# Kernel tuning notes

Measured on AMD Instinct MI355X. Metric: run time of the kernel, lower is better.

The kernel has to match this reference:

```python
import jax, jax.numpy as jnp
import numpy as np

B, N, D, H = 512, 200, 128, 8
DH = D // H
CLIP = 10.0
NEG = -1e9


def setup_inputs():
    ks = jax.random.split(jax.random.key(0), 10)
    s = 1.0 / float(np.sqrt(D))
    f32 = jnp.float32
    return {
        "x": jax.random.normal(ks[0], (2, B, N, N), f32),
        "rf": jax.random.uniform(ks[1], (B, 2), f32),
        "node_embeddings": jax.random.normal(ks[2], (B, N, D), f32),
        "graph_embedding": jax.random.normal(ks[3], (B, D), f32),
        "Wk1_w": jax.random.normal(ks[4], (D, D), f32) * s,
        "Wk1_b": jnp.zeros((D,), f32),
        "Wv_w": jax.random.normal(ks[5], (D, D), f32) * s,
        "Wk2_w": jax.random.normal(ks[6], (D, D), f32) * s,
        "Wout_w": jax.random.normal(ks[7], (D, D), f32) * s,
        "Wq_w": jax.random.normal(ks[8], (D, D + 2), f32) * s,
        "init_node": jnp.zeros((D,), f32),
    }


def _forward(x, rf, node_embeddings, Wk1_w, Wk1_b, Wv_w, Wk2_w, Wout_w, Wq_w, init_node):
    # static projections (compute_static)
    K1 = node_embeddings @ Wk1_w.T + Wk1_b  # [B,N,D]
    V = node_embeddings @ Wv_w.T
    K2 = node_embeddings @ Wk2_w.T
    K1h = K1.reshape(B, N, H, DH).transpose(0, 2, 1, 3)  # [B,H,N,DH]
    Vh = V.reshape(B, N, H, DH).transpose(0, 2, 1, 3)
    barange = jnp.arange(B)
    narange = jnp.arange(N)

    def step(carry, _):
        mask, ctx, end = carry  # mask [B,N] bool, ctx [B,2+D], end [B] bool
        Q1 = ctx @ Wq_w.T  # [B,D]  (Wq_step)
        qh = Q1.reshape(B, H, DH)
        scores = jnp.einsum('bhd,bhnd->bhn', qh, K1h) / jnp.sqrt(jnp.float32(DH))
        scores = jnp.where(mask[:, None, :], NEG, scores)
        attn = jax.nn.softmax(scores, axis=-1)
        mha = jnp.einsum('bhn,bhnd->bhd', attn, Vh).reshape(B, D)
        Q2 = mha @ Wout_w.T  # [B,D]
        logits = CLIP * jnp.tanh(jnp.einsum('bd,bnd->bn', Q2, K2) / jnp.sqrt(jnp.float32(D)))
        logits = jnp.where(mask, NEG, logits)
        log_p = jax.nn.log_softmax(logits, axis=-1)  # [B,N]
        nxt = jnp.argmax(log_p, axis=-1)  # greedy decode (deterministic)
        nxt = jnp.where(end, nxt, 0)  # once node 0 chosen, stay at 0
        cur_emb = node_embeddings[barange, nxt]  # [B,D]
        end = end & (nxt != 0)
        mask = mask | (narange[None, :] == nxt[:, None])
        ctx = jnp.concatenate([rf, cur_emb], axis=1)
        return (mask, ctx, end), (log_p, nxt)

    ctx0 = jnp.concatenate([rf, jnp.broadcast_to(init_node, (B, D))], axis=1)
    carry0 = (jnp.zeros((B, N), bool), ctx0, jnp.ones((B,), bool))
    _, (log_ps, tours) = jax.lax.scan(step, carry0, None, length=N)
    log_ps = log_ps.transpose(1, 0, 2)  # [B,N,N]
    pi = tours.T  # [B,N]

    # get_cost
    index = jnp.argmax(pi == 0, axis=1)  # first occurrence of stop node 0
    steps_mask = narange[None, :] < index[:, None]
    cols = pi * steps_mask
    sol = jnp.zeros((B, N), jnp.float32).at[barange[:, None], cols].set(1.0)
    f1 = jnp.einsum('bn,bnm,bm->b', sol, x[0], sol)[:, None, None]  # [B,1,1]
    f2 = jnp.einsum('bn,bnm,bm->b', sol, x[1], sol)[:, None, None]
    cost = -(f1 * rf[0, 0] + f2 * rf[0, 1]).squeeze()  # [B]

    # log-likelihood of tour, weighted by solution membership
    chosen = jnp.take_along_axis(log_ps, pi[:, :, None], axis=2)[:, :, 0]  # [B,N]
    w = jnp.take_along_axis(sol, pi, axis=1)
    ll = jnp.sum(chosen * w, axis=1)  # [B]
    return cost, f1, f2, ll, pi


def reference(x, rf, node_embeddings, graph_embedding, Wk1_w, Wk1_b, Wv_w, Wk2_w, Wout_w, Wq_w, init_node):
    return _forward(x, rf, node_embeddings, Wk1_w, Wk1_b, Wv_w, Wk2_w, Wout_w, Wq_w, init_node)
```

## Files before the change

### kernel.cpp

```cpp
#include <hip/hip_runtime.h>
#include <math.h>

#define NEGV (-1e9f)

#define OUT_F   0l
#define M_F     52428800l
#define QR_F    (M_F + 65536l)
#define QI_F    (QR_F + 65536l)
#define SOL_F   (QI_F + 65536l)
#define WS_FLOATS (SOL_F + 102400l)

typedef float f32x4 __attribute__((ext_vector_type(4)));

#define DPPF(x, ctrl, oldv) __int_as_float(__builtin_amdgcn_update_dpp( \
      __float_as_int(oldv), __float_as_int(x), ctrl, 0xF, 0xF, false))

__device__ __forceinline__ float wave_max(float x) {
  x = fmaxf(x, DPPF(x, 0x111, -INFINITY));
  x = fmaxf(x, DPPF(x, 0x112, -INFINITY));
  x = fmaxf(x, DPPF(x, 0x114, -INFINITY));
  x = fmaxf(x, DPPF(x, 0x118, -INFINITY));
  x = fmaxf(x, DPPF(x, 0x142, -INFINITY));
  x = fmaxf(x, DPPF(x, 0x143, -INFINITY));
  return __int_as_float(__builtin_amdgcn_readlane(__float_as_int(x), 63));
}
__device__ __forceinline__ float wave_sum(float x) {
  x = x + DPPF(x, 0x111, 0.f);
  x = x + DPPF(x, 0x112, 0.f);
  x = x + DPPF(x, 0x114, 0.f);
  x = x + DPPF(x, 0x118, 0.f);
  x = x + DPPF(x, 0x142, 0.f);
  x = x + DPPF(x, 0x143, 0.f);
  return __int_as_float(__builtin_amdgcn_readlane(__float_as_int(x), 63));
}

__global__ __launch_bounds__(256)
void build_M(const float* __restrict__ Wk1, const float* __restrict__ Wv,
             const float* __restrict__ Wk2, const float* __restrict__ Wout,
             const float* __restrict__ Wq, float* __restrict__ Mbuf) {
  int g = blockIdx.x * 256 + threadIdx.x;
  int j = g >> 9, c = g & 511;
  float val;
  if (c < 128) {
    val = Wk1[c * 128 + j];
  } else if (c < 256) {
    val = Wv[(c - 128) * 128 + j];
  } else if (c < 384) {
    int d = c - 256;
    float s = 0.f;
    for (int e = 0; e < 128; ++e) s += Wk2[e * 128 + j] * Wout[e * 128 + d];
    val = s;
  } else {
    val = Wq[(c - 384) * 130 + 2 + j];
  }
  Mbuf[j * 512 + c] = val;
}

__global__ __launch_bounds__(256)
void build_Q(const float* __restrict__ rf, const float* __restrict__ Wq,
             const float* __restrict__ initn, float* __restrict__ QR,
             float* __restrict__ QI, int* __restrict__ ctr) {
  int g = blockIdx.x * 256 + threadIdx.x;
  if (g == 0) *ctr = 0;
  int b = g >> 7, d = g & 127;
  float qr = Wq[d * 130 + 0] * rf[b * 2 + 0] + Wq[d * 130 + 1] * rf[b * 2 + 1];
  float qi = qr;
  for (int j = 0; j < 128; ++j) qi += Wq[d * 130 + 2 + j] * initn[j];
  QR[g] = qr;
  QI[g] = qi;
}

__global__ __launch_bounds__(256)
void gemm_static(const float* __restrict__ emb, const float* __restrict__ Mbuf,
                 const float* __restrict__ bk1, const float* __restrict__ QR,
                 float* __restrict__ OUT) {
  int bid = blockIdx.x;
  int lo = bid & 7, hi = bid >> 3;
  int rt = lo + 8 * (hi % 200);
  int ct = hi / 200;
  int r0 = rt * 64, c0 = ct * 64;
  int t = threadIdx.x, ty = t >> 4, tx = t & 15;
  int row0 = r0 + ty * 4;
  int col  = c0 + tx * 4;
  float acc[4][4] = {};
  const float* mp = Mbuf + col;
  for (int kb = 0; kb < 32; ++kb) {
    int k = kb * 4;
    float4 b0 = *(const float4*)(mp + (long)(k + 0) * 512);
    float4 b1 = *(const float4*)(mp + (long)(k + 1) * 512);
    float4 b2 = *(const float4*)(mp + (long)(k + 2) * 512);
    float4 b3 = *(const float4*)(mp + (long)(k + 3) * 512);
    float bm[4][4] = {{b0.x,b0.y,b0.z,b0.w},{b1.x,b1.y,b1.z,b1.w},
                      {b2.x,b2.y,b2.z,b2.w},{b3.x,b3.y,b3.z,b3.w}};
    #pragma unroll
    for (int rr = 0; rr < 4; ++rr) {
      float4 a4 = *(const float4*)(emb + (long)(row0 + rr) * 128 + k);
      float av[4] = {a4.x, a4.y, a4.z, a4.w};
      #pragma unroll
      for (int i = 0; i < 4; ++i)
        #pragma unroll
        for (int cc = 0; cc < 4; ++cc)
          acc[rr][cc] += av[i] * bm[i][cc];
    }
  }
  float badd[4] = {0.f, 0.f, 0.f, 0.f};
  if (c0 < 128) {
    #pragma unroll
    for (int cc = 0; cc < 4; ++cc) badd[cc] = bk1[col + cc];
  }
  #pragma unroll
  for (int rr = 0; rr < 4; ++rr) {
    int row = row0 + rr;
    float v[4];
    #pragma unroll
    for (int cc = 0; cc < 4; ++cc) v[cc] = acc[rr][cc] + badd[cc];
    if (col >= 384) {
      int bb = row / 200;
      #pragma unroll
      for (int cc = 0; cc < 4; ++cc) v[cc] += QR[bb * 128 + (col - 384) + cc];
    }
    float4 v4; v4.x = v[0]; v4.y = v[1]; v4.z = v[2]; v4.w = v[3];
    *(float4*)(OUT + (long)row * 512 + col) = v4;
  }
}

__global__ void init_ctr(int* __restrict__ c) { *c = 0; }

__global__ __attribute__((amdgpu_flat_work_group_size(512, 512), amdgpu_waves_per_eu(2, 2)))
void decode512(const float* __restrict__ OUT, const float* __restrict__ QI,
               const float* __restrict__ x, const float* __restrict__ rf,
               int* __restrict__ ctr, float* __restrict__ out) {
  __shared__ __align__(16) float qall[201 * 128];
  __shared__ float sc[1600];
  __shared__ __align__(16) float mhal[128];
  __shared__ float lg[200];
  __shared__ float sb[200];
  __shared__ float redc[16];
  __shared__ int bsel;

  const int t = threadIdx.x;
  const int lane = t & 63, wave = t >> 6;
  const int o = t >> 2, r4 = t & 3;
  const int mn = t >> 1, half = t & 1;
  const int vst  = (r4 == 0) ? 0 : (r4 == 1 ? 48 : (r4 == 2 ? 100 : 152));
  const bool mid = (r4 == 1) || (r4 == 2);

  float kreg[64], ureg[64], vreg[52];

  for (;;) {
    if (t == 0) bsel = atomicAdd(ctr, 1);
    __syncthreads();
    const int b = bsel;
    if (b >= 512) break;
    const float* outb = OUT + (long)b * 200 * 512;

    for (int f = t; f < 25728; f += 512) {
      int row = f >> 7, d = f & 127;
      qall[f] = (row < 200) ? outb[row * 512 + 384 + d] : QI[b * 128 + d];
    }
    #pragma unroll
    for (int k = 0; k < 4; ++k) {
      int n = lane + 64 * k;
      if (n < 200) {
        const float* kp = outb + n * 512 + wave * 16;
        #pragma unroll
        for (int c = 0; c < 4; ++c)
          *(f32x4*)&kreg[k * 16 + c * 4] = *(const f32x4*)(kp + c * 4);
      } else {
        #pragma unroll
        for (int c = 0; c < 16; ++c) kreg[k * 16 + c] = 0.f;
      }
    }
    if (t < 400) {
      const float* up = outb + mn * 512 + 256 + 64 * half;
      #pragma unroll
      for (int c = 0; c < 16; ++c)
        *(f32x4*)&ureg[c * 4] = *(const f32x4*)(up + c * 4);
    }
    {
      const float* vp = outb + 128 + o;
      #pragma unroll
      for (int i = 0; i < 48; ++i) vreg[i] = vp[(vst + i) * 512];
      vreg[48] = mid ? vp[(vst + 48) * 512] : 0.f;
      vreg[49] = mid ? vp[(vst + 49) * 512] : 0.f;
      vreg[50] = mid ? vp[(vst + 50) * 512] : 0.f;
      vreg[51] = mid ? vp[(vst + 51) * 512] : 0.f;
    }

    int cur = 200;
    int mk = 0;
    bool cmb = false;
    bool live = true, picked0 = false;
    float llsum = 0.f, chose = 0.f;

    __syncthreads();

    for (int st = 0; st < 200; ++st) {
      {
        const float* qb = qall + cur * 128 + wave * 16;
        f32x4 q0 = *(const f32x4*)(qb + 0);
        f32x4 q1 = *(const f32x4*)(qb + 4);
        f32x4 q2 = *(const f32x4*)(qb + 8);
        f32x4 q3 = *(const f32x4*)(qb + 12);
        float sv[4];
        float mx = -INFINITY;
        #pragma unroll
        for (int k = 0; k < 4; ++k) {
          int n = lane + 64 * k;
          float s = -INFINITY;
          if (n < 200) {
            float a = q0[0] * kreg[k * 16 + 0];
            a += q0[1] * kreg[k * 16 + 1];
            a += q0[2] * kreg[k * 16 + 2];
            a += q0[3] * kreg[k * 16 + 3];
            a += q1[0] * kreg[k * 16 + 4];
            a += q1[1] * kreg[k * 16 + 5];
            a += q1[2] * kreg[k * 16 + 6];
            a += q1[3] * kreg[k * 16 + 7];
            a += q2[0] * kreg[k * 16 + 8];
            a += q2[1] * kreg[k * 16 + 9];
            a += q2[2] * kreg[k * 16 + 10];
            a += q2[3] * kreg[k * 16 + 11];
            a += q3[0] * kreg[k * 16 + 12];
            a += q3[1] * kreg[k * 16 + 13];
            a += q3[2] * kreg[k * 16 + 14];
            a += q3[3] * kreg[k * 16 + 15];
            s = a * 0.25f;
            if (mk & (1 << k)) s = NEGV;
          }
          sv[k] = s;
          mx = fmaxf(mx, s);
        }
        float vmax = wave_max(mx);
        float ls = 0.f;
        #pragma unroll
        for (int k = 0; k < 4; ++k) { sv[k] = expf(sv[k] - vmax); ls += sv[k]; }
        ls = wave_sum(ls);
        #pragma unroll
        for (int k = 0; k < 4; ++k) {
          int n = lane + 64 * k;
          if (n < 200) sc[wave * 200 + n] = sv[k] / ls;
        }
      }

      {
        const float* ap = sc + wave * 200 + vst;
        float ac[4] = {0.f, 0.f, 0.f, 0.f};
        #pragma unroll
        for (int c = 0; c < 12; ++c) {
          f32x4 av = *(const f32x4*)(ap + c * 4);
          float s = av[0] * vreg[c * 4 + 0];
          s += av[1] * vreg[c * 4 + 1];
          s += av[2] * vreg[c * 4 + 2];
          s += av[3] * vreg[c * 4 + 3];
          ac[c & 3] += s;
        }
        if (mid) {
          f32x4 av = *(const f32x4*)(ap + 48);
          float s = av[0] * vreg[48];
          s += av[1] * vreg[49]; s += av[2] * vreg[50]; s += av[3] * vreg[51];
          ac[0] += s;
        }
        float a = (ac[0] + ac[1]) + (ac[2] + ac[3]);
        a += DPPF(a, 0xB1, 0.f);
        a += DPPF(a, 0x4E, 0.f);
        if (r4 == 0) mhal[o] = a;
      }
      __syncthreads();

      if (t < 400) {
        float ac[4] = {0.f, 0.f, 0.f, 0.f};
        #pragma unroll
        for (int c = 0; c < 16; ++c) {
          f32x4 mh = *(const f32x4*)&mhal[64 * half + c * 4];
          float s = mh[0] * ureg[c * 4 + 0];
          s += mh[1] * ureg[c * 4 + 1];
          s += mh[2] * ureg[c * 4 + 2];
          s += mh[3] * ureg[c * 4 + 3];
          ac[c & 3] += s;
        }
        float a = (ac[0] + ac[1]) + (ac[2] + ac[3]);
        a += DPPF(a, 0xB1, 0.f);
        if (half == 0) {
          float l = 10.f * tanhf(a / 11.313708498984761f);
          lg[mn] = cmb ? NEGV : l;
        }
      }
      __syncthreads();

      int nxt;
      {
        float lv[4];
        float mx = -INFINITY;
        #pragma unroll
        for (int k = 0; k < 4; ++k) {
          int n = lane + 64 * k;
          lv[k] = (n < 200) ? lg[n] : -INFINITY;
          mx = fmaxf(mx, lv[k]);
        }
        float vmax = wave_max(mx);
        int bidx = -1;
        #pragma unroll
        for (int k = 0; k < 4; ++k) {
          unsigned long long bm =
              __ballot((lane + 64 * k < 200) && (lv[k] == vmax));
          if (bidx < 0 && bm != 0ull) bidx = k * 64 + (int)__builtin_ctzll(bm);
        }
        nxt = live ? bidx : 0;
        if (wave == 7) {
          float e = 0.f;
          #pragma unroll
          for (int k = 0; k < 4; ++k) e += expf(lv[k] - vmax);
          float se_ = wave_sum(e);
          float lse = logf(se_);
          if (t == 448) {
            chose = live ? (-lse) : ((lv[0] - vmax) - lse);
            out[2048 + (long)b * 200 + st] = (float)nxt;
          }
        }
      }

      if (!live) {
        if (t == 448) llsum += chose * (float)(200 - st);
        for (int s2 = st + 1 + t; s2 < 200; s2 += 512)
          out[2048 + (long)b * 200 + s2] = 0.f;
        break;
      }
      if (t == 448) llsum += chose;
      if ((nxt & 63) == lane) mk |= 1 << (nxt >> 6);
      if (t < 400 && nxt == mn) cmb = true;
      cur = nxt;
      if (nxt == 0) { live = false; picked0 = true; }
    }

    if (t == 448) out[1536 + b] = picked0 ? llsum : 0.f;
    if (t < 400 && half == 0) {
      float s = (mn == 0) ? 1.f : ((picked0 && cmb) ? 1.f : 0.f);
      sb[mn] = s;
    }
    __syncthreads();

    {
      const int c2 = t >> 1, hf = t & 1;
      float a1 = 0.f, a2 = 0.f;
      if (c2 < 200) {
        const float* xp0 = x + (long)b * 40000 + hf * 20000 + c2;
        const float* xp1 = x + 20480000l + (long)b * 40000 + hf * 20000 + c2;
        #pragma unroll 4
        for (int i = 0; i < 100; ++i) {
          float w2 = sb[hf * 100 + i];
          a1 += xp0[i * 200] * w2;
          a2 += xp1[i * 200] * w2;
        }
      }
      a1 += DPPF(a1, 0xB1, 0.f);
      a2 += DPPF(a2, 0xB1, 0.f);
      if (hf == 0 && c2 < 200) {
        float w = sb[c2];
        a1 *= w; a2 *= w;
      } else {
        a1 = 0.f; a2 = 0.f;
      }
      a1 = wave_sum(a1);
      a2 = wave_sum(a2);
      if (lane == 0) { redc[wave * 2] = a1; redc[wave * 2 + 1] = a2; }
      __syncthreads();
      if (t == 0) {
        float f1 = ((redc[0] + redc[2]) + (redc[4] + redc[6])) +
                   ((redc[8] + redc[10]) + (redc[12] + redc[14]));
        float f2 = ((redc[1] + redc[3]) + (redc[5] + redc[7])) +
                   ((redc[9] + redc[11]) + (redc[13] + redc[15]));
        out[b]        = -(f1 * rf[0] + f2 * rf[1]);
        out[512 + b]  = f1;
        out[1024 + b] = f2;
      }
    }
    __syncthreads();
  }
}

__global__ __attribute__((amdgpu_flat_work_group_size(1024, 1024)))
void decode(const float* __restrict__ OUT, const float* __restrict__ QI,
            int* __restrict__ ctr, float* __restrict__ sol,
            float* __restrict__ out) {
  __shared__ __align__(16) float k1r[25600];
  __shared__ __align__(16) float at[1600];
  __shared__ __align__(16) float mhal[128];
  __shared__ float lg[200];
  __shared__ __align__(16) float qv[128];
  __shared__ __align__(16) float ul[12800];
  __shared__ int   bci;
  __shared__ int   bsel;

  const int t = threadIdx.x;
  const int lane = t & 63, wave = t >> 6;
  const int o = t >> 3, q8 = t & 7;
  const int m4 = t >> 2, j4 = t & 3;
  const int stq = (q8 * 25) & ~3;
  const int cq  = ((((q8 + 1) * 25) & ~3) - stq) >> 2;

  for (;;) {
    if (t == 0) bsel = atomicAdd(ctr, 1);
    __syncthreads();
    const int b = bsel;
    if (b >= 512) break;
    const float* outb = OUT + (long)b * 200 * 512;

    for (int p = 0; p < 25; ++p) {
      int f = p * 1024 + t;
      int n = f >> 7, d = f & 127;
      k1r[n * 128 + ((d + 4 * n) & 127)] = outb[n * 512 + d];
    }
    for (int f = t; f < 12800; f += 1024) {
      int m = f >> 6, c = f & 63;
      ul[m * 64 + ((c + 4 * m) & 63)] =
          outb[m * 512 + 256 + (c >> 4) * 32 + 16 + (c & 15)];
    }
    f32x4 vA = {}, vB = {}, vC = {}, vD = {}, vE = {}, vF = {}, vG = {};
    {
      const float* vp = outb + 128 + o;
      #pragma unroll
      for (int e = 0; e < 4; ++e) vA[e] = vp[(stq + 0 + e) * 512];
      #pragma unroll
      for (int e = 0; e < 4; ++e) vB[e] = vp[(stq + 4 + e) * 512];
      #pragma unroll
      for (int e = 0; e < 4; ++e) vC[e] = vp[(stq + 8 + e) * 512];
      #pragma unroll
      for (int e = 0; e < 4; ++e) vD[e] = vp[(stq + 12 + e) * 512];
      #pragma unroll
      for (int e = 0; e < 4; ++e) vE[e] = vp[(stq + 16 + e) * 512];
      #pragma unroll
      for (int e = 0; e < 4; ++e) vF[e] = vp[(stq + 20 + e) * 512];
      if (cq == 7) {
        #pragma unroll
        for (int e = 0; e < 4; ++e) vG[e] = vp[(stq + 24 + e) * 512];
      }
    }
    f32x4 urR0 = {}, urR1 = {}, urR2 = {}, urR3 = {};
    if (t < 800) {
      const float* up = outb + m4 * 512 + 256 + j4 * 32;
      urR0 = *(const f32x4*)(up + 4 * ((0 + j4) & 3));
      urR1 = *(const f32x4*)(up + 4 * ((1 + j4) & 3));
      urR2 = *(const f32x4*)(up + 4 * ((2 + j4) & 3));
      urR3 = *(const f32x4*)(up + 4 * ((3 + j4) & 3));
    }
    if (t < 128) qv[t] = QI[b * 128 + t];

    int mk = 0;
    bool cm = false;
    bool live = true, picked0 = false;
    float llsum = 0.f, chose = 0.f;

    __syncthreads();

    for (int st = 0; st < 200; ++st) {
      if (wave < 8) {
        const int hb = wave * 16;
        float acc[4] = {};
        #pragma unroll
        for (int hf = 0; hf < 2; ++hf) {
          f32x4 qa = *(const f32x4*)&qv[hb + hf * 8];
          f32x4 qb2 = *(const f32x4*)&qv[hb + hf * 8 + 4];
          #pragma unroll
          for (int k = 0; k < 4; ++k) {
            int n = lane + 64 * k;
            if (n < 200) {
              const float* kb = k1r + n * 128;
              int off  = (hb + hf * 8 + 4 * n) & 127;
              int off2 = (hb + hf * 8 + 4 + 4 * n) & 127;
              f32x4 kA = *(const f32x4*)(kb + off);
              f32x4 kB = *(const f32x4*)(kb + off2);
              float ah = qa[0] * kA[0];
              ah += qa[1] * kA[1]; ah += qa[2] * kA[2]; ah += qa[3] * kA[3];
              ah += qb2[0] * kB[0]; ah += qb2[1] * kB[1];
              ah += qb2[2] * kB[2]; ah += qb2[3] * kB[3];
              acc[k] += ah;
            }
          }
        }
        float sv[4];
        float mx = -INFINITY;
        #pragma unroll
        for (int k = 0; k < 4; ++k) {
          int n = lane + 64 * k;
          float s = -INFINITY;
          if (n < 200) {
            s = acc[k] * 0.25f;
            if (mk & (1 << k)) s = NEGV;
          }
          sv[k] = s;
          mx = fmaxf(mx, s);
        }
        float vmax = wave_max(mx);
        float ls = 0.f;
        #pragma unroll
        for (int k = 0; k < 4; ++k) { sv[k] = expf(sv[k] - vmax); ls += sv[k]; }
        ls = wave_sum(ls);
        #pragma unroll
        for (int k = 0; k < 4; ++k) {
          int n = lane + 64 * k;
          if (n < 200) at[wave * 200 + n] = sv[k] / ls;
        }
      }
      __syncthreads();

      {
        const int h2 = t >> 7;
        const float* ap = at + h2 * 200 + stq;
        float a = 0.f;
        f32x4 av;
        av = *(const f32x4*)(ap + 0);
        a += av[0]*vA[0]; a += av[1]*vA[1]; a += av[2]*vA[2]; a += av[3]*vA[3];
        av = *(const f32x4*)(ap + 4);
        a += av[0]*vB[0]; a += av[1]*vB[1]; a += av[2]*vB[2]; a += av[3]*vB[3];
        av = *(const f32x4*)(ap + 8);
        a += av[0]*vC[0]; a += av[1]*vC[1]; a += av[2]*vC[2]; a += av[3]*vC[3];
        av = *(const f32x4*)(ap + 12);
        a += av[0]*vD[0]; a += av[1]*vD[1]; a += av[2]*vD[2]; a += av[3]*vD[3];
        av = *(const f32x4*)(ap + 16);
        a += av[0]*vE[0]; a += av[1]*vE[1]; a += av[2]*vE[2]; a += av[3]*vE[3];
        av = *(const f32x4*)(ap + 20);
        a += av[0]*vF[0]; a += av[1]*vF[1]; a += av[2]*vF[2]; a += av[3]*vF[3];
        if (cq == 7) {
          av = *(const f32x4*)(ap + 24);
          a += av[0]*vG[0]; a += av[1]*vG[1]; a += av[2]*vG[2]; a += av[3]*vG[3];
        }
        a += DPPF(a, 0xB1, 0.f);
        a += DPPF(a, 0x4E, 0.f);
        a += DPPF(a, 0x141, 0.f);
        if (q8 == 0) mhal[o] = a;
      }
      __syncthreads();

      if (t < 800) {
        float a = 0.f;
        {
          f32x4 ml;
          ml = *(const f32x4*)&mhal[j4 * 32 + ((0 + j4) & 3) * 4];
          a += ml[0]*urR0[0]; a += ml[1]*urR0[1]; a += ml[2]*urR0[2]; a += ml[3]*urR0[3];
          ml = *(const f32x4*)&mhal[j4 * 32 + ((1 + j4) & 3) * 4];
          a += ml[0]*urR1[0]; a += ml[1]*urR1[1]; a += ml[2]*urR1[2]; a += ml[3]*urR1[3];
          ml = *(const f32x4*)&mhal[j4 * 32 + ((2 + j4) & 3) * 4];
          a += ml[0]*urR2[0]; a += ml[1]*urR2[1]; a += ml[2]*urR2[2]; a += ml[3]*urR2[3];
          ml = *(const f32x4*)&mhal[j4 * 32 + ((3 + j4) & 3) * 4];
          a += ml[0]*urR3[0]; a += ml[1]*urR3[1]; a += ml[2]*urR3[2]; a += ml[3]*urR3[3];
        }
        const int ubase = m4 * 64;
        #pragma unroll
        for (int c = 0; c < 4; ++c) {
          int ci = (c + j4) & 3;
          f32x4 mh = *(const f32x4*)&mhal[j4 * 32 + 16 + ci * 4];
          f32x4 uu = *(const f32x4*)&ul[ubase + ((j4 * 16 + ci * 4 + 4 * m4) & 63)];
          a += mh[0]*uu[0]; a += mh[1]*uu[1]; a += mh[2]*uu[2]; a += mh[3]*uu[3];
        }
        a += DPPF(a, 0xB1, 0.f);
        a += DPPF(a, 0x4E, 0.f);
        if (j4 == 0) {
          float l = 10.f * tanhf(a / 11.313708498984761f);
          lg[m4] = cm ? NEGV : l;
        }
      }
      __syncthreads();

      if (wave < 8) {
        float lv[4];
        float mx = -INFINITY;
        #pragma unroll
        for (int k = 0; k < 4; ++k) {
          int n = lane + 64 * k;
          lv[k] = (n < 200) ? lg[n] : -INFINITY;
          mx = fmaxf(mx, lv[k]);
        }
        float vmax = wave_max(mx);
        int bidx = -1;
        #pragma unroll
        for (int k = 0; k < 4; ++k) {
          unsigned long long bm =
              __ballot((lane + 64 * k < 200) && (lv[k] == vmax));
          if (bidx < 0 && bm != 0ull) bidx = k * 64 + (int)__builtin_ctzll(bm);
        }
        int nxt = live ? bidx : 0;
        if (t < 128) qv[t] = outb[(long)nxt * 512 + 384 + t];
        float e = 0.f;
        #pragma unroll
        for (int k = 0; k < 4; ++k) e += expf(lv[k] - vmax);
        float se_ = wave_sum(e);
        float lse = logf(se_);
        if (t == 0) {
          chose = live ? (-lse) : ((lv[0] - vmax) - lse);
          out[2048 + (long)b * 200 + st] = (float)nxt;
          bci = nxt;
        }
      }
      __syncthreads();

      int nxt = bci;
      if (!live) {
        if (t == 0) llsum += chose * (float)(200 - st);
        for (int s2 = st + 1 + t; s2 < 200; s2 += 1024)
          out[2048 + (long)b * 200 + s2] = 0.f;
        break;
      }
      if (t == 0) llsum += chose;
      if (wave < 8 && (nxt & 63) == lane) mk |= 1 << (nxt >> 6);
      if (t < 800 && nxt == m4) cm = true;
      if (nxt == 0) { live = false; picked0 = true; }
    }

    if (t == 0) out[1536 + b] = picked0 ? llsum : 0.f;
    if (t < 800 && j4 == 0) {
      float s = (m4 == 0) ? 1.f : ((picked0 && cm) ? 1.f : 0.f);
      sol[(long)b * 200 + m4] = s;
    }
    __syncthreads();
  }
}

__global__ __launch_bounds__(256)
void cost_kernel(const float* __restrict__ x, const float* __restrict__ rf,
                 const float* __restrict__ sol, float* __restrict__ out) {
  __shared__ float solL[256];
  __shared__ float red[8];
  const int b = blockIdx.x, t = threadIdx.x;
  solL[t] = (t < 200) ? sol[b * 200 + t] : 0.f;
  __syncthreads();
  const float* x0 = x + (long)b * 40000;
  const float* x1 = x + 20480000l + (long)b * 40000;
  float a1 = 0.f, a2 = 0.f;
  if (t < 200) {
    #pragma unroll 4
    for (int i = 0; i < 200; ++i) {
      float w2 = solL[i];
      a1 += x0[i * 200 + t] * w2;
      a2 += x1[i * 200 + t] * w2;
    }
    float w = solL[t];
    a1 *= w; a2 *= w;
  }
  #pragma unroll
  for (int off = 32; off > 0; off >>= 1) {
    a1 += __shfl_xor(a1, off);
    a2 += __shfl_xor(a2, off);
  }
  if ((t & 63) == 0) { red[(t >> 6) * 2] = a1; red[(t >> 6) * 2 + 1] = a2; }
  __syncthreads();
  if (t == 0) {
    float f1 = red[0] + red[2] + red[4] + red[6];
    float f2 = red[1] + red[3] + red[5] + red[7];
    out[b]        = -(f1 * rf[0] + f2 * rf[1]);
    out[512 + b]  = f1;
    out[1024 + b] = f2;
  }
}

extern "C" void kernel_launch(void* const* d_in, const int* in_sizes, int n_in,
                              void* d_out, int out_size, void* d_ws, size_t ws_size,
                              hipStream_t stream) {
  const float* x     = (const float*)d_in[0];
  const float* rf    = (const float*)d_in[1];
  const float* emb   = (const float*)d_in[2];
  const float* Wk1   = (const float*)d_in[4];
  const float* bk1   = (const float*)d_in[5];
  const float* Wv    = (const float*)d_in[6];
  const float* Wk2   = (const float*)d_in[7];
  const float* Wout  = (const float*)d_in[8];
  const float* Wq    = (const float*)d_in[9];
  const float* initn = (const float*)d_in[10];
  float* out = (float*)d_out;
  float* ws  = (float*)d_ws;

  if (ws_size < (size_t)WS_FLOATS * 4) return;

  float* OUTb = ws + OUT_F;
  float* Mb   = ws + M_F;
  float* QRb  = ws + QR_F;
  float* QIb  = ws + QI_F;
  float* solb = ws + SOL_F;
  int*   ctrb = (int*)(ws + QR_F);

  ctrb = (int*)(ws + SOL_F + 102400l - 4l);
  ctrb = (int*)(ws + M_F);

  build_M<<<256, 256, 0, stream>>>(Wk1, Wv, Wk2, Wout, Wq, Mb);
  build_Q<<<256, 256, 0, stream>>>(rf, Wq, initn, QRb, QIb, (int*)(ws + QI_F + 65536l - 4l));
  gemm_static<<<12800, 256, 0, stream>>>(emb, Mb, bk1, QRb, OUTb);
  init_ctr<<<1, 1, 0, stream>>>(ctrb);

  hipFuncAttributes fa;
  bool big = false;
  if (hipFuncGetAttributes(&fa, (const void*)decode512) == hipSuccess)
    big = (fa.localSizeBytes <= 64);
  if (big) {
    decode512<<<256, 512, 0, stream>>>(OUTb, QIb, x, rf, ctrb, out);
  } else {
    decode<<<256, 1024, 0, stream>>>(OUTb, QIb, ctrb, solb, out);
    cost_kernel<<<512, 256, 0, stream>>>(x, rf, solb, out);
  }
}
```

Before: 1.198 ms.

## Drop shared query staging; load next-step query rows from global, launch 512 blocks

Removes the roughly 100 KB shared-memory array that staged all query rows per batch element. Each step now loads the selected node's 16-float query slice straight from global memory into registers, right after the argmax. With the shared footprint gone, more workgroups can be resident per CU, and the grid is doubled to 512 persistent blocks to use that. The cost is a dependent global load on each step's critical path, and the register pressure may change. The host also drops the stale counter initialisation that build_Q used to do.

```diff
diff --git a/kernel.cpp b/kernel.cpp
--- a/kernel.cpp
+++ b/kernel.cpp
@@ -59,9 +59,8 @@
 __global__ __launch_bounds__(256)
 void build_Q(const float* __restrict__ rf, const float* __restrict__ Wq,
              const float* __restrict__ initn, float* __restrict__ QR,
-             float* __restrict__ QI, int* __restrict__ ctr) {
+             float* __restrict__ QI) {
   int g = blockIdx.x * 256 + threadIdx.x;
-  if (g == 0) *ctr = 0;
   int b = g >> 7, d = g & 127;
   float qr = Wq[d * 130 + 0] * rf[b * 2 + 0] + Wq[d * 130 + 1] * rf[b * 2 + 1];
   float qi = qr;
@@ -69,6 +68,8 @@
   QR[g] = qr;
   QI[g] = qi;
 }
+
+__global__ void init_ctr(int* __restrict__ c) { *c = 0; }
 
 __global__ __launch_bounds__(256)
 void gemm_static(const float* __restrict__ emb, const float* __restrict__ Mbuf,
@@ -124,13 +125,10 @@
   }
 }
 
-__global__ void init_ctr(int* __restrict__ c) { *c = 0; }
-
 __global__ __attribute__((amdgpu_flat_work_group_size(512, 512), amdgpu_waves_per_eu(2, 2)))
 void decode512(const float* __restrict__ OUT, const float* __restrict__ QI,
                const float* __restrict__ x, const float* __restrict__ rf,
                int* __restrict__ ctr, float* __restrict__ out) {
-  __shared__ __align__(16) float qall[201 * 128];
   __shared__ float sc[1600];
   __shared__ __align__(16) float mhal[128];
   __shared__ float lg[200];
@@ -154,10 +152,6 @@
     if (b >= 512) break;
     const float* outb = OUT + (long)b * 200 * 512;
 
-    for (int f = t; f < 25728; f += 512) {
-      int row = f >> 7, d = f & 127;
-      qall[f] = (row < 200) ? outb[row * 512 + 384 + d] : QI[b * 128 + d];
-    }
     #pragma unroll
     for (int k = 0; k < 4; ++k) {
       int n = lane + 64 * k;
@@ -186,8 +180,15 @@
       vreg[50] = mid ? vp[(vst + 50) * 512] : 0.f;
       vreg[51] = mid ? vp[(vst + 51) * 512] : 0.f;
     }
-
-    int cur = 200;
+    f32x4 q0, q1, q2, q3;
+    {
+      const float* qp = QI + b * 128 + wave * 16;
+      q0 = *(const f32x4*)(qp + 0);
+      q1 = *(const f32x4*)(qp + 4);
+      q2 = *(const f32x4*)(qp + 8);
+      q3 = *(const f32x4*)(qp + 12);
+    }
+
     int mk = 0;
     bool cmb = false;
     bool live = true, picked0 = false;
@@ -197,11 +198,6 @@
 
     for (int st = 0; st < 200; ++st) {
       {
-        const float* qb = qall + cur * 128 + wave * 16;
-        f32x4 q0 = *(const f32x4*)(qb + 0);
-        f32x4 q1 = *(const f32x4*)(qb + 4);
-        f32x4 q2 = *(const f32x4*)(qb + 8);
-        f32x4 q3 = *(const f32x4*)(qb + 12);
         float sv[4];
         float mx = -INFINITY;
         #pragma unroll
@@ -307,6 +303,11 @@
           if (bidx < 0 && bm != 0ull) bidx = k * 64 + (int)__builtin_ctzll(bm);
         }
         nxt = live ? bidx : 0;
+        const float* qp = outb + (long)nxt * 512 + 384 + wave * 16;
+        q0 = *(const f32x4*)(qp + 0);
+        q1 = *(const f32x4*)(qp + 4);
+        q2 = *(const f32x4*)(qp + 8);
+        q3 = *(const f32x4*)(qp + 12);
         if (wave == 7) {
           float e = 0.f;
           #pragma unroll
@@ -329,7 +330,6 @@
       if (t == 448) llsum += chose;
       if ((nxt & 63) == lane) mk |= 1 << (nxt >> 6);
       if (t < 400 && nxt == mn) cmb = true;
-      cur = nxt;
       if (nxt == 0) { live = false; picked0 = true; }
     }
 
@@ -676,13 +676,10 @@
   float* QRb  = ws + QR_F;
   float* QIb  = ws + QI_F;
   float* solb = ws + SOL_F;
-  int*   ctrb = (int*)(ws + QR_F);
-
-  ctrb = (int*)(ws + SOL_F + 102400l - 4l);
-  ctrb = (int*)(ws + M_F);
+  int* ctrb = (int*)(ws + M_F);
 
   build_M<<<256, 256, 0, stream>>>(Wk1, Wv, Wk2, Wout, Wq, Mb);
-  build_Q<<<256, 256, 0, stream>>>(rf, Wq, initn, QRb, QIb, (int*)(ws + QI_F + 65536l - 4l));
+  build_Q<<<256, 256, 0, stream>>>(rf, Wq, initn, QRb, QIb);
   gemm_static<<<12800, 256, 0, stream>>>(emb, Mb, bk1, QRb, OUTb);
   init_ctr<<<1, 1, 0, stream>>>(ctrb);
 
@@ -691,7 +688,7 @@
   if (hipFuncGetAttributes(&fa, (const void*)decode512) == hipSuccess)
     big = (fa.localSizeBytes <= 64);
   if (big) {
-    decode512<<<256, 512, 0, stream>>>(OUTb, QIb, x, rf, ctrb, out);
+    decode512<<<512, 512, 0, stream>>>(OUTb, QIb, x, rf, ctrb, out);
   } else {
     decode<<<256, 1024, 0, stream>>>(OUTb, QIb, ctrb, solb, out);
     cost_kernel<<<512, 256, 0, stream>>>(x, rf, solb, out);
```

After: 1.213 ms. No clear change (+1.3%).
